# Performance work log

Measured on AMD Instinct MI355X. Metric: run time of the kernel, lower is better.

## Reference

```python
import jax, jax.numpy as jnp
import numpy as np
from itertools import combinations

A = 4          # anchor_points
K = 16         # neighbor_num
INTRA = A * (A - 1) // 2   # 6
CH = INTRA * 2 + A * A     # 28 = generator channels
B, N, S = 1, 8192, 4096
CIN, COUT = 64, 128


def cdist(x):
    # pairwise euclidean distances [B,N,N], zero-safe sqrt (zero grad at d=0)
    sq = jnp.sum(x * x, -1)
    d2 = sq[:, :, None] + sq[:, None, :] - 2.0 * jnp.einsum('bnc,bmc->bnm', x, x)
    d2 = jnp.maximum(d2, 0.0)
    m = d2 > 0
    return jnp.where(m, jnp.sqrt(jnp.where(m, d2, 1.0)), 0.0)


def index_points(points, idx):
    # points [B,N,...], idx [B,*] -> [B,*,...]
    return jax.vmap(lambda p, i: p[i])(points, idx)


def index_points_dists(dists, i1, i2):
    # dists [B,N,N]; result[b,...] = dists[b, i1[b,...], i2[b,...]]
    i1, i2 = jnp.broadcast_arrays(i1, i2)
    return jax.vmap(lambda d, a, b: d[a, b])(dists, i1, i2)


def generator(xyz):
    # RotationInvariantDistFea.forward(xyz, concat_raw_relative_fea=True)
    D = cdist(xyz)
    neg_nd, ni = jax.lax.top_k(-D, K)   # K >= A; smallest-K, sorted ascending
    nd = -neg_nd
    ai = ni[:, :, :A]
    # intra-anchor dists: dists to anchors 1..A-1 plus pairwise dists among them
    subs = [index_points_dists(D, ai[:, :, pi], ai[:, :, pj])[:, :, None]
            for pi, pj in combinations(range(1, A), 2)]
    intra = jnp.concatenate([nd[:, :, 1:A]] + subs, axis=2)  # [B,P,6]
    # inter-anchor dists: center anchors x neighbor anchors -> [B,P,K,A*A]
    nai = index_points(ai, ni)                                # [B,P,K,A]
    inter = index_points_dists(D, ai[:, :, None, :, None],
                               nai[:, :, :, None, :]).reshape(D.shape[0], D.shape[1], K, A * A)
    center = jnp.broadcast_to(intra[:, :, None, :], (intra.shape[0], intra.shape[1], K, INTRA))
    rf = jnp.concatenate([center, index_points(intra, ni), inter], axis=3)  # [B,P,K,28]
    return rf, ni, D


def mlp(x, W, b, g, be, act):
    # Linear + BatchNorm1d (training mode: stats over batch*points) + optional leaky_relu(0.2)
    y = x @ W + b
    mu = jnp.mean(y, (0, 1))
    var = jnp.var(y, (0, 1))
    y = (y - mu) * jax.lax.rsqrt(var + 1e-5) * g + be
    return jax.nn.leaky_relu(y, 0.2) if act else y


def forward(xyz, feature, sample_indexes, Ww, bw, gw, betaw, Wb, bb, gb, betab, Wo, bo, go, betao):
    rf_before, ni_before, D_before = generator(xyz)
    intra_before = rf_before[:, :, 0, :INTRA]
    xyz_s = index_points(xyz, sample_indexes)
    feat = index_points(feature, sample_indexes)
    intra_before = index_points(intra_before, sample_indexes)
    rf_after, ni_after, _ = generator(xyz_s)
    intra_after = rf_after[:, :, 0, :INTRA]
    a_before = index_points(ni_before[:, :, :A], sample_indexes)                  # [B,S,A]
    a_after = jax.vmap(lambda s, a: s[a])(sample_indexes, ni_after[:, :, :A])     # map to global idx
    inter = index_points_dists(D_before, a_before[:, :, :, None],
                               a_after[:, :, None, :]).reshape(B, S, A * A)
    adf = jnp.concatenate([intra_before, intra_after, inter], axis=2)             # [B,S,28]
    w = mlp(adf, Ww, bw, gw, betaw, False)
    bia = mlp(adf, Wb, bb, gb, betab, False)
    feat = jax.nn.leaky_relu(feat * w + bia, 0.2)
    feat = jnp.concatenate([feat, adf], axis=2)                                   # [B,S,92]
    feat = mlp(feat, Wo, bo, go, betao, True)                                     # [B,S,128]
    return xyz_s, feat, rf_after, ni_after


def setup_inputs():
    key = jax.random.key(0)
    ks = jax.random.split(key, 8)
    xyz = jax.random.normal(ks[0], (B, N, 3), jnp.float32)
    feature = jax.random.normal(ks[1], (B, N, CIN), jnp.float32)
    sample_indexes = jnp.stack([jax.random.permutation(jax.random.fold_in(ks[2], i), N)[:S]
                                for i in range(B)]).astype(jnp.int32)

    def lin(k, cin, cout):
        k1, k2 = jax.random.split(k)
        W = jax.random.normal(k1, (cin, cout), jnp.float32) / np.float32(np.sqrt(cin))
        b = jax.random.normal(k2, (cout,), jnp.float32) * 0.01
        return W, b, jnp.ones((cout,), jnp.float32), jnp.zeros((cout,), jnp.float32)

    Ww, bw, gw, betaw = lin(ks[5], CH, CIN)
    Wb, bb, gb, betab = lin(ks[6], CH, CIN)
    Wo, bo, go, betao = lin(ks[7], CH + CIN, COUT)
    return dict(xyz=xyz, feature=feature, sample_indexes=sample_indexes,
                Ww=Ww, bw=bw, gw=gw, betaw=betaw,
                Wb=Wb, bb=bb, gb=gb, betab=betab,
                Wo=Wo, bo=bo, go=go, betao=betao)


def reference(xyz, feature, sample_indexes, Ww, bw, gw, betaw, Wb, bb, gb, betab, Wo, bo, go, betao):
    return forward(xyz, feature, sample_indexes, Ww, bw, gw, betaw, Wb, bb, gb, betab, Wo, bo, go, betao)
```

## Files before the change

kernel.cpp:

```cpp
#include <hip/hip_runtime.h>
#include <hip/hip_bf16.h>
#include <math.h>

#define N_PTS 8192
#define S_PTS 4096
typedef unsigned long long u64;
typedef unsigned u32;

__device__ __forceinline__ float d2_f32_gram(const float4 a, const float4 b) {
    float dot = __fadd_rn(__fadd_rn(__fmul_rn(a.x, b.x), __fmul_rn(a.y, b.y)),
                          __fmul_rn(a.z, b.z));
    float d2 = __fsub_rn(__fadd_rn(a.w, b.w), __fmul_rn(2.0f, dot));
    return fmaxf(d2, 0.0f);
}

__device__ __forceinline__ float pair_dist_f(const float4 a, const float4 b) {
    float d2 = d2_f32_gram(a, b);
    return d2 > 0.0f ? __fsqrt_rn(d2) : 0.0f;
}

__global__ __launch_bounds__(256) void stage_kernel(
        const float* __restrict__ xyz, const int* __restrict__ sidx,
        float4* __restrict__ cb, float4* __restrict__ ca,
        float* __restrict__ out_xyz_s) {
    int i = blockIdx.x * blockDim.x + threadIdx.x;
    if (i < N_PTS) {
        float x = xyz[i * 3 + 0], y = xyz[i * 3 + 1], z = xyz[i * 3 + 2];
        float sq = __fadd_rn(__fadd_rn(__fmul_rn(x, x), __fmul_rn(y, y)),
                             __fmul_rn(z, z));
        cb[i] = make_float4(x, y, z, sq);
    }
    if (i < S_PTS) {
        int si = sidx[i];
        float x = xyz[si * 3 + 0], y = xyz[si * 3 + 1], z = xyz[si * 3 + 2];
        float sq = __fadd_rn(__fadd_rn(__fmul_rn(x, x), __fmul_rn(y, y)),
                             __fmul_rn(z, z));
        ca[i] = make_float4(x, y, z, sq);
        out_xyz_s[i * 3 + 0] = x;
        out_xyz_s[i * 3 + 1] = y;
        out_xyz_s[i * 3 + 2] = z;
    }
}


template <int KOUT, int ITERS>
__device__ u64 knn_full_ladder(const float4 q, const float4* __restrict__ cand,
                               int lane) {
    u32 Lk[KOUT], Li[KOUT];
#pragma unroll
    for (int j = 0; j < KOUT; ++j) { Lk[j] = 0xFFFFFFFFu; Li[j] = 0xFFFFFFFFu; }
    int c = lane;
    for (int tt = 0; tt < ITERS; ++tt, c += 64) {
        float d2 = d2_f32_gram(q, cand[c]);
        float Df = d2 > 0.0f ? __fsqrt_rn(d2) : 0.0f;
        u32 kb = __float_as_uint(Df);
        if (kb < Lk[KOUT - 1]) {
#pragma unroll
            for (int j = KOUT - 1; j >= 1; --j) {
                bool up = kb < Lk[j - 1], ins = kb < Lk[j];
                Lk[j] = up ? Lk[j - 1] : (ins ? kb : Lk[j]);
                Li[j] = up ? Li[j - 1] : (ins ? (u32)c : Li[j]);
            }
            bool i0 = kb < Lk[0];
            Lk[0] = i0 ? kb : Lk[0];
            Li[0] = i0 ? (u32)c : Li[0];
        }
    }
    u64 Lu[KOUT];
#pragma unroll
    for (int j = 0; j < KOUT; ++j) Lu[j] = ((u64)Lk[j] << 32) | (u64)Li[j];
    u64 res = ~0ull;
#pragma unroll
    for (int r = 0; r < KOUT; ++r) {
        u64 m = Lu[0];
#pragma unroll
        for (int off = 32; off >= 1; off >>= 1) {
            u64 o = __shfl_xor(m, off, 64);
            m = (o < m) ? o : m;
        }
        if (lane == r) res = m;
        if (Lu[0] == m) {
#pragma unroll
            for (int j = 0; j < KOUT - 1; ++j) Lu[j] = Lu[j + 1];
            Lu[KOUT - 1] = ~0ull;
        }
    }
    return res;
}

template <int K, int NC>
__device__ u64 final_select(const float4 qq, const float4* __restrict__ cand,
                            const u64* bufq, u32 cnt, int lane) {
    if (cnt <= 64u) {
        u64 v = (lane < (int)cnt) ? bufq[lane] : ~0ull;
#pragma unroll
        for (int k = 2; k <= 64; k <<= 1) {
#pragma unroll
            for (int j2 = k >> 1; j2 >= 1; j2 >>= 1) {
                u64 o = __shfl_xor(v, j2, 64);
                bool keepMin = (((lane & j2) == 0) == ((lane & k) == 0));
                bool less = o < v;
                v = keepMin ? (less ? o : v) : (less ? v : o);
            }
        }
        return v;
    } else if (cnt <= 256u) {
        u64 L0 = ~0ull, L1 = ~0ull, L2 = ~0ull, L3 = ~0ull;
        for (u32 mm = lane; mm < cnt; mm += 64) {
            u64 kk = bufq[mm];
            if (kk < L3) {
                if (kk < L1) {
                    L3 = L2; L2 = L1;
                    if (kk < L0) { L1 = L0; L0 = kk; } else L1 = kk;
                } else {
                    if (kk < L2) { L3 = L2; L2 = kk; } else L3 = kk;
                }
            }
        }
        u64 res = ~0ull;
#pragma unroll
        for (int r = 0; r < K; ++r) {
            u64 mr = L0;
#pragma unroll
            for (int off = 32; off >= 1; off >>= 1) {
                u64 o = __shfl_xor(mr, off, 64);
                mr = (o < mr) ? o : mr;
            }
            if (lane == r) res = mr;
            if (L0 == mr) { L0 = L1; L1 = L2; L2 = L3; L3 = ~0ull; }
        }
        return res;
    }
    return knn_full_ladder<K, NC / 64>(qq, cand, lane);
}

template <int J, int K, int NC, int Q>
__device__ __forceinline__ u64 knn_selectq(
        const float4* qs, const float4* __restrict__ cand, int t,
        u32* mins, u64* buf, u32* shm) {
    int lane = t & 63, wid = t >> 6;
    u32 d2b[Q][J];
    u32 m[Q];
#pragma unroll
    for (int qi = 0; qi < Q; ++qi) m[qi] = 0xFFFFFFFFu;
#pragma unroll
    for (int j = 0; j < J; ++j) {
        float4 c = cand[t + 256 * j];
#pragma unroll
        for (int qi = 0; qi < Q; ++qi) {
            u32 b = __float_as_uint(d2_f32_gram(qs[qi], c));
            d2b[qi][j] = b;
            m[qi] = b < m[qi] ? b : m[qi];
        }
    }
#pragma unroll
    for (int qi = 0; qi < Q; ++qi) mins[qi * 256 + t] = m[qi];
    __syncthreads();
    if (wid < Q) {
        const u32* mq = mins + wid * 256;
        u32 v = mq[lane];
        u32 v2 = mq[lane + 64];  v = v2 < v ? v2 : v;
        v2 = mq[lane + 128];     v = v2 < v ? v2 : v;
        v2 = mq[lane + 192];     v = v2 < v ? v2 : v;
#pragma unroll
        for (int k = 2; k <= 64; k <<= 1) {
#pragma unroll
            for (int j2 = k >> 1; j2 >= 1; j2 >>= 1) {
                u32 o = __shfl_xor(v, j2, 64);
                bool keepMin = (((lane & j2) == 0) == ((lane & k) == 0));
                bool less = o < v;
                v = keepMin ? (less ? o : v) : (less ? v : o);
            }
        }
        if (lane == K - 1) shm[wid] = v;
    }
    __syncthreads();
    u32 tau[Q], c[Q], x[Q];
#pragma unroll
    for (int qi = 0; qi < Q; ++qi) {
        tau[qi] = shm[qi];
        u32 cc = 0;
#pragma unroll
        for (int j = 0; j < J; ++j) cc += (d2b[qi][j] <= tau[qi]) ? 1u : 0u;
        c[qi] = cc;
        u32 xx = cc;
#pragma unroll
        for (int off = 1; off < 64; off <<= 1) {
            u32 y = __shfl_up(xx, off, 64);
            if (lane >= off) xx += y;
        }
        x[qi] = xx;
        if (lane == 63) shm[Q + qi * 4 + wid] = xx;
    }
    __syncthreads();
    u32 cnt[Q];
#pragma unroll
    for (int qi = 0; qi < Q; ++qi) {
        u32 base = x[qi] - c[qi];
        for (int w = 0; w < wid; ++w) base += shm[Q + qi * 4 + w];
        cnt[qi] = shm[Q + qi * 4 + 0] + shm[Q + qi * 4 + 1] +
                  shm[Q + qi * 4 + 2] + shm[Q + qi * 4 + 3];
        if (cnt[qi] <= 256u) {
            u32 off = base;
#pragma unroll
            for (int j = 0; j < J; ++j) {
                if (d2b[qi][j] <= tau[qi]) {
                    float d2 = __uint_as_float(d2b[qi][j]);
                    float D = d2 > 0.0f ? __fsqrt_rn(d2) : 0.0f;
                    buf[qi * 256 + off++] = ((u64)__float_as_uint(D) << 32) |
                                            (u64)(u32)(t + 256 * j);
                }
            }
        }
    }
    __syncthreads();
    u64 res = ~0ull;
#pragma unroll
    for (int qi = 0; qi < Q; ++qi)
        if (wid == qi)
            res = final_select<K, NC>(qs[qi], cand, buf + qi * 256, cnt[qi], lane);
    return res;
}

__global__ __launch_bounds__(256, 4) void knn_kernel(
        const float4* __restrict__ cb, const float4* __restrict__ ca,
        const int* __restrict__ sidx,
        int* __restrict__ a_before, float* __restrict__ intra_before,
        int* __restrict__ ni_i, float* __restrict__ intra_after,
        float* __restrict__ out_ni) {
    __shared__ u32 mins[4 * 256];
    __shared__ u64 buf[4 * 256];
    __shared__ u32 shm[24];
    int t = threadIdx.x, lane = t & 63, wid = t >> 6;
    int bid = blockIdx.x;
    if (bid < S_PTS / 4) {
        int s0 = bid * 4;
        float4 qs[4];
#pragma unroll
        for (int qi = 0; qi < 4; ++qi) qs[qi] = ca[s0 + qi];
        u64 res = knn_selectq<16, 16, 4096, 4>(qs, ca, t, mins, buf, shm);
        if (wid < 4) {
            int s = s0 + wid;
            int idx = (int)(res & 0xffffffffull);
            if (lane < 16) {
                ni_i[s * 16 + lane] = idx;
                out_ni[s * 16 + lane] = (float)idx;
            }
            if (lane >= 1 && lane < 4)
                intra_after[s * 6 + (lane - 1)] =
                    __uint_as_float((u32)(res >> 32));
            int i1 = __shfl(idx, 1, 64);
            int i2 = __shfl(idx, 2, 64);
            int i3 = __shfl(idx, 3, 64);
            if (lane < 3) {
                int pa = (lane == 2) ? i2 : i1;
                int pb = (lane == 0) ? i2 : i3;
                intra_after[s * 6 + 3 + lane] = pair_dist_f(ca[pa], ca[pb]);
            }
        }
    } else {
        int s0 = (bid - S_PTS / 4) * 2;
        float4 qs[2];
        qs[0] = cb[sidx[s0]];
        qs[1] = cb[sidx[s0 + 1]];
        u64 res = knn_selectq<32, 4, 8192, 2>(qs, cb, t, mins, buf, shm);
        if (wid < 2) {
            int s = s0 + wid;
            int idx = (int)(res & 0xffffffffull);
            if (lane < 4) a_before[s * 4 + lane] = idx;
            if (lane >= 1 && lane < 4)
                intra_before[s * 6 + (lane - 1)] =
                    __uint_as_float((u32)(res >> 32));
            int i1 = __shfl(idx, 1, 64);
            int i2 = __shfl(idx, 2, 64);
            int i3 = __shfl(idx, 3, 64);
            if (lane < 3) {
                int pa = (lane == 2) ? i2 : i1;
                int pb = (lane == 0) ? i2 : i3;
                intra_before[s * 6 + 3 + lane] = pair_dist_f(cb[pa], cb[pb]);
            }
        }
    }
}

__global__ __launch_bounds__(256) void assemble_kernel(
        const float4* __restrict__ ca, const float4* __restrict__ cb,
        const int* __restrict__ ni_i, const float* __restrict__ intra_after,
        const int* __restrict__ a_before, const float* __restrict__ intra_before,
        const int* __restrict__ sidx,
        float* __restrict__ out_rf, float* __restrict__ adf) {
    __shared__ int s_ni[4][16];
    __shared__ float s_rf[4][16 * 28];
    __shared__ float s_ia[4][8];
    int t = threadIdx.x, wid = t >> 6, lane = t & 63;
    int s = blockIdx.x * 4 + wid;
    if (lane < 16) s_ni[wid][lane] = ni_i[s * 16 + lane];
    if (lane < 6) s_ia[wid][lane] = intra_after[s * 6 + lane];
    __syncthreads();

    int k = lane >> 2, qq = lane & 3;
    int nai_q = ni_i[s_ni[wid][k] * 16 + qq];
    float4 pq = ca[nai_q];
#pragma unroll
    for (int p = 0; p < 4; ++p) {
        float4 pp = ca[s_ni[wid][p]];
        s_rf[wid][k * 28 + 12 + p * 4 + qq] = pair_dist_f(pp, pq);
    }
    for (int idx = lane; idx < 16 * 12; idx += 64) {
        int kk = idx / 12, c = idx % 12;
        float v = (c < 6) ? s_ia[wid][c] : intra_after[s_ni[wid][kk] * 6 + (c - 6)];
        s_rf[wid][kk * 28 + c] = v;
    }
    if (lane < 16) {
        int p = lane >> 2, q2 = lane & 3;
        int ib = a_before[s * 4 + p];
        int ia = sidx[s_ni[wid][q2]];
        adf[s * 28 + 12 + lane] = pair_dist_f(cb[ib], cb[ia]);
    } else if (lane >= 32 && lane < 38) {
        adf[s * 28 + (lane - 32)] = intra_before[s * 6 + (lane - 32)];
    } else if (lane >= 40 && lane < 46) {
        adf[s * 28 + 6 + (lane - 40)] = s_ia[wid][lane - 40];
    }
    __syncthreads();
    const int base = s * 16 * 28;
    for (int idx = lane; idx < 16 * 28; idx += 64) out_rf[base + idx] = s_rf[wid][idx];
}

__global__ __launch_bounds__(256) void mlp1_kernel(
        const float* __restrict__ adf,
        const float* __restrict__ Ww, const float* __restrict__ bw,
        const float* __restrict__ Wb, const float* __restrict__ bb,
        float* __restrict__ y_wb,
        float* __restrict__ part1, float* __restrict__ part2) {
    __shared__ float sW[28 * 128];
    __shared__ float sb[128];
    __shared__ float sA[32 * 28];
    __shared__ float red[32][128];
    int t = threadIdx.x;
    for (int i = t; i < 28 * 128; i += 256) {
        int k = i >> 7, c = i & 127;
        sW[i] = (c < 64) ? Ww[k * 64 + c] : Wb[k * 64 + (c - 64)];
    }
    if (t < 128) sb[t] = (t < 64) ? bw[t] : bb[t - 64];
    int s0 = blockIdx.x * 32;
    for (int i = t; i < 32 * 28; i += 256) sA[i] = adf[s0 * 28 + i];
    __syncthreads();
    int sl = t >> 3, grp = t & 7;
    int s = s0 + sl;
    float acc[16];
#pragma unroll
    for (int k = 0; k < 16; ++k) acc[k] = sb[grp * 16 + k];
    for (int k2 = 0; k2 < 28; ++k2) {
        float a = sA[sl * 28 + k2];
#pragma unroll
        for (int k = 0; k < 16; ++k)
            acc[k] = fmaf(a, sW[k2 * 128 + grp * 16 + k], acc[k]);
    }
#pragma unroll
    for (int k = 0; k < 16; ++k) {
        y_wb[(grp * 16 + k) * 4096 + s] = acc[k];
        red[sl][grp * 16 + k] = acc[k];
    }
    __syncthreads();
    if (t < 128) {
        float s1 = 0.0f, s2 = 0.0f;
#pragma unroll 8
        for (int r = 0; r < 32; ++r) {
            float v = red[r][t];
            s1 += v;
            s2 = fmaf(v, v, s2);
        }
        part1[blockIdx.x * 128 + t] = s1;
        part2[blockIdx.x * 128 + t] = s2;
    }
}

__global__ __launch_bounds__(256) void mlp2_kernel(
        const float* __restrict__ y_wb,
        const float* __restrict__ part1, const float* __restrict__ part2,
        const float* __restrict__ gw, const float* __restrict__ betaw,
        const float* __restrict__ gb, const float* __restrict__ betab,
        const float* __restrict__ feature, const int* __restrict__ sidx,
        const float* __restrict__ adf,
        const float* __restrict__ Wo, const float* __restrict__ bo,
        float* __restrict__ y_o) {
    __shared__ float sW[92 * 128];
    __shared__ float t2[16 * 129];
    __shared__ float scat[16 * 92];
    __shared__ float s_sc[128], s_sh[128];
    int t = threadIdx.x;
    int s0 = blockIdx.x * 16;
    if (t < 128) {
        float s1 = 0.0f, s2 = 0.0f;
        for (int b = 0; b < 128; ++b) {
            s1 += part1[b * 128 + t];
            s2 += part2[b * 128 + t];
        }
        float mean = s1 * (1.0f / 4096.0f);
        float var = s2 * (1.0f / 4096.0f) - mean * mean;
        float g = (t < 64) ? gw[t] : gb[t - 64];
        float be = (t < 64) ? betaw[t] : betab[t - 64];
        float sc = g / sqrtf(var + 1e-5f);
        s_sc[t] = sc;
        s_sh[t] = be - mean * sc;
    }
    for (int i = t; i < 92 * 128; i += 256) sW[i] = Wo[i];
    __syncthreads();
    for (int i = t; i < 16 * 128; i += 256) {
        int row = i & 15, c = i >> 4;
        t2[row * 129 + c] = fmaf(y_wb[c * 4096 + s0 + row], s_sc[c], s_sh[c]);
    }
    __syncthreads();
    for (int rr = 0; rr < 16; rr += 4) {
        int r = rr + (t >> 6);
        int c = t & 63;
        int si = sidx[s0 + r];
        float f = feature[si * 64 + c];
        float v = fmaf(f, t2[r * 129 + c], t2[r * 129 + 64 + c]);
        scat[r * 92 + c] = v >= 0.0f ? v : 0.2f * v;
    }
    for (int i = t; i < 16 * 28; i += 256) {
        int row = i / 28, k = i % 28;
        scat[row * 92 + 64 + k] = adf[(s0 + row) * 28 + k];
    }
    __syncthreads();
    int r = t >> 4, cg = t & 15;
    float acc[8];
#pragma unroll
    for (int j = 0; j < 8; ++j) acc[j] = bo[cg * 8 + j];
    for (int c = 0; c < 92; ++c) {
        float a = scat[r * 92 + c];
#pragma unroll
        for (int j = 0; j < 8; ++j)
            acc[j] = fmaf(a, sW[c * 128 + cg * 8 + j], acc[j]);
    }
    int s = s0 + r;
#pragma unroll
    for (int j = 0; j < 8; ++j) y_o[(cg * 8 + j) * 4096 + s] = acc[j];
}

__global__ __launch_bounds__(256) void stats_final_kernel(
        const float* __restrict__ y_o,
        const float* __restrict__ go, const float* __restrict__ betao,
        float* __restrict__ out_feat) {
    int c = blockIdx.x;
    const float* p = y_o + c * 4096;
    float s1 = 0.0f, s2 = 0.0f;
    for (int i = threadIdx.x; i < 4096; i += 256) {
        float v = p[i];
        s1 += v;
        s2 = fmaf(v, v, s2);
    }
    __shared__ float l1[256], l2[256];
    __shared__ float s_sc, s_sh;
    l1[threadIdx.x] = s1;
    l2[threadIdx.x] = s2;
    __syncthreads();
    for (int off = 128; off; off >>= 1) {
        if (threadIdx.x < off) {
            l1[threadIdx.x] += l1[threadIdx.x + off];
            l2[threadIdx.x] += l2[threadIdx.x + off];
        }
        __syncthreads();
    }
    if (threadIdx.x == 0) {
        float mean = l1[0] * (1.0f / 4096.0f);
        float var = l2[0] * (1.0f / 4096.0f) - mean * mean;
        float sc = go[c] / sqrtf(var + 1e-5f);
        s_sc = sc;
        s_sh = betao[c] - mean * sc;
    }
    __syncthreads();
    float sc = s_sc, sh = s_sh;
    for (int i = threadIdx.x; i < 4096; i += 256) {
        float v = fmaf(p[i], sc, sh);
        v = v >= 0.0f ? v : 0.2f * v;
        out_feat[i * 128 + c] = v;
    }
}

extern "C" void kernel_launch(void* const* d_in, const int* in_sizes, int n_in,
                              void* d_out, int out_size, void* d_ws, size_t ws_size,
                              hipStream_t stream) {
    const float* xyz = (const float*)d_in[0];
    const float* feature = (const float*)d_in[1];
    const int* sidx = (const int*)d_in[2];
    const float* Ww = (const float*)d_in[3];
    const float* bw = (const float*)d_in[4];
    const float* gw = (const float*)d_in[5];
    const float* betaw = (const float*)d_in[6];
    const float* Wb = (const float*)d_in[7];
    const float* bb = (const float*)d_in[8];
    const float* gb = (const float*)d_in[9];
    const float* betab = (const float*)d_in[10];
    const float* Wo = (const float*)d_in[11];
    const float* bo = (const float*)d_in[12];
    const float* go = (const float*)d_in[13];
    const float* betao = (const float*)d_in[14];

    float* out = (float*)d_out;
    float* out_xyz = out;
    float* out_feat = out + 12288;
    float* out_rf = out + 12288 + 524288;
    float* out_ni = out + 12288 + 524288 + 1835008;

    float* ws = (float*)d_ws;
    float4* cb = (float4*)ws;
    float4* ca = (float4*)(ws + 32768);
    int* a_before = (int*)(ws + 49152);
    float* intra_before = ws + 65536;
    int* ni_i = (int*)(ws + 90112);
    float* intra_after = ws + 155648;
    float* adf = ws + 180224;
    float* y_wb = ws + 294912;
    float* y_o = ws + 819200;
    float* part1 = ws + 1343488;
    float* part2 = ws + 1359872;

    stage_kernel<<<32, 256, 0, stream>>>(xyz, sidx, cb, ca, out_xyz);
    knn_kernel<<<S_PTS / 4 + S_PTS / 2, 256, 0, stream>>>(
        cb, ca, sidx, a_before, intra_before, ni_i, intra_after, out_ni);
    assemble_kernel<<<1024, 256, 0, stream>>>(ca, cb, ni_i, intra_after, a_before,
                                              intra_before, sidx, out_rf, adf);
    mlp1_kernel<<<128, 256, 0, stream>>>(adf, Ww, bw, Wb, bb, y_wb, part1, part2);
    mlp2_kernel<<<256, 256, 0, stream>>>(y_wb, part1, part2, gw, betaw, gb, betab,
                                         feature, sidx, adf, Wo, bo, y_o);
    stats_final_kernel<<<128, 256, 0, stream>>>(y_o, go, betao, out_feat);
}
```

Baseline: 161.7 us.

## Split before-sample kNN over point halves with four queries per block and merge

The 4-NN search over all 8192 points used to run two queries per block over the full set. Each block now handles four queries over one 4096-point half, reusing the same templated selection path as the after-sample kNN. A new small kernel merges the two sorted top-4 lists with a bitonic-style network and computes the intra-anchor distances. This raises reuse of loaded candidate points across queries, at the cost of one extra kernel launch and a staging buffer.

Result: slower. 166.9 us (+3.2%).

```diff
diff --git a/kernel.cpp b/kernel.cpp
--- a/kernel.cpp
+++ b/kernel.cpp
@@ -225,7 +225,7 @@
 __global__ __launch_bounds__(256, 4) void knn_kernel(
         const float4* __restrict__ cb, const float4* __restrict__ ca,
         const int* __restrict__ sidx,
-        int* __restrict__ a_before, float* __restrict__ intra_before,
+        u64* __restrict__ stage_b4,
         int* __restrict__ ni_i, float* __restrict__ intra_after,
         float* __restrict__ out_ni) {
     __shared__ u32 mins[4 * 256];
@@ -259,28 +259,56 @@
             }
         }
     } else {
-        int s0 = (bid - S_PTS / 4) * 2;
-        float4 qs[2];
-        qs[0] = cb[sidx[s0]];
-        qs[1] = cb[sidx[s0 + 1]];
-        u64 res = knn_selectq<32, 4, 8192, 2>(qs, cb, t, mins, buf, shm);
-        if (wid < 2) {
+        int idx2 = bid - S_PTS / 4;
+        int qg = idx2 >> 1;
+        int h = idx2 & 1;
+        int s0 = qg * 4;
+        float4 qs[4];
+#pragma unroll
+        for (int qi = 0; qi < 4; ++qi) qs[qi] = cb[sidx[s0 + qi]];
+        u64 res = knn_selectq<16, 4, 4096, 4>(qs, cb + h * 4096, t, mins, buf, shm);
+        if (wid < 4 && lane < 4) {
             int s = s0 + wid;
-            int idx = (int)(res & 0xffffffffull);
-            if (lane < 4) a_before[s * 4 + lane] = idx;
-            if (lane >= 1 && lane < 4)
-                intra_before[s * 6 + (lane - 1)] =
-                    __uint_as_float((u32)(res >> 32));
-            int i1 = __shfl(idx, 1, 64);
-            int i2 = __shfl(idx, 2, 64);
-            int i3 = __shfl(idx, 3, 64);
-            if (lane < 3) {
-                int pa = (lane == 2) ? i2 : i1;
-                int pb = (lane == 0) ? i2 : i3;
-                intra_before[s * 6 + 3 + lane] = pair_dist_f(cb[pa], cb[pb]);
-            }
-        }
-    }
+            stage_b4[s * 8 + h * 4 + lane] = res + (u64)(h * 4096);
+        }
+    }
+}
+
+__device__ __forceinline__ void cswap_u64(u64& x, u64& y) {
+    u64 lo = x < y ? x : y;
+    u64 hi = x < y ? y : x;
+    x = lo; y = hi;
+}
+
+__global__ __launch_bounds__(256) void merge_before_kernel(
+        const u64* __restrict__ stage_b4, const float4* __restrict__ cb,
+        int* __restrict__ a_before, float* __restrict__ intra_before) {
+    int s = blockIdx.x * 256 + threadIdx.x;
+    const u64* p = stage_b4 + s * 8;
+    u64 a0 = p[0], a1 = p[1], a2 = p[2], a3 = p[3];
+    u64 b0 = p[4], b1 = p[5], b2 = p[6], b3 = p[7];
+    u64 c0 = a0 < b3 ? a0 : b3;
+    u64 c1 = a1 < b2 ? a1 : b2;
+    u64 c2 = a2 < b1 ? a2 : b1;
+    u64 c3 = a3 < b0 ? a3 : b0;
+    cswap_u64(c0, c1); cswap_u64(c2, c3);
+    cswap_u64(c0, c2); cswap_u64(c1, c3);
+    cswap_u64(c1, c2);
+    int i0 = (int)(c0 & 0xffffffffull);
+    int i1 = (int)(c1 & 0xffffffffull);
+    int i2 = (int)(c2 & 0xffffffffull);
+    int i3 = (int)(c3 & 0xffffffffull);
+    a_before[s * 4 + 0] = i0;
+    a_before[s * 4 + 1] = i1;
+    a_before[s * 4 + 2] = i2;
+    a_before[s * 4 + 3] = i3;
+    intra_before[s * 6 + 0] = __uint_as_float((u32)(c1 >> 32));
+    intra_before[s * 6 + 1] = __uint_as_float((u32)(c2 >> 32));
+    intra_before[s * 6 + 2] = __uint_as_float((u32)(c3 >> 32));
+    float4 p1 = cb[i1], p2 = cb[i2], p3 = cb[i3];
+    intra_before[s * 6 + 3] = pair_dist_f(p1, p2);
+    intra_before[s * 6 + 4] = pair_dist_f(p1, p3);
+    intra_before[s * 6 + 5] = pair_dist_f(p2, p3);
 }
 
 __global__ __launch_bounds__(256) void assemble_kernel(
@@ -516,10 +544,13 @@
     float* y_o = ws + 819200;
     float* part1 = ws + 1343488;
     float* part2 = ws + 1359872;
+    u64* stage_b4 = (u64*)(ws + 1376256);
 
     stage_kernel<<<32, 256, 0, stream>>>(xyz, sidx, cb, ca, out_xyz);
-    knn_kernel<<<S_PTS / 4 + S_PTS / 2, 256, 0, stream>>>(
-        cb, ca, sidx, a_before, intra_before, ni_i, intra_after, out_ni);
+    knn_kernel<<<S_PTS / 4 + 2048, 256, 0, stream>>>(
+        cb, ca, sidx, stage_b4, ni_i, intra_after, out_ni);
+    merge_before_kernel<<<16, 256, 0, stream>>>(stage_b4, cb, a_before,
+                                                intra_before);
     assemble_kernel<<<1024, 256, 0, stream>>>(ca, cb, ni_i, intra_after, a_before,
                                               intra_before, sidx, out_rf, adf);
     mlp1_kernel<<<128, 256, 0, stream>>>(adf, Ww, bw, Wb, bb, y_wb, part1, part2);
```
